# Optimization experiments

Hardware: AMD Instinct MI355X
Metric: run time of the kernel (lower is better)

The kernel has to match this reference:

```python
import jax, jax.numpy as jnp
import numpy as np
from jax import lax

B, C, L = 32, 8, 4096
K, S = 128, 64  # num_shapelets, shapelets_size


def setup_inputs() -> dict:
    key = jax.random.key(0)
    kx, ks = jax.random.split(key)
    x = jax.random.normal(kx, (B, C, L), dtype=jnp.float32)
    shapelets = jax.random.normal(ks, (C, K, S), dtype=jnp.float32)
    return {"x": x, "shapelets": shapelets}


def reference(x, shapelets):
    # x: (B, C, L); shapelets: (C, K, S)
    # Equivalent to: unfold -> cdist(p=2) -> sum over channels -> min over windows.
    # Use the ||a-b||^2 = ||a||^2 + ||b||^2 - 2 a.b expansion so the unfolded
    # (B, C, W, S) tensor is never materialized; cross-terms via grouped conv.
    Bc, Cc, Lc = x.shape
    _, Kc, Sc = shapelets.shape
    dn = ("NCH", "OIH", "NCH")
    # cross[b, c*K+k, w] = sum_s x[b,c,w+s] * shapelets[c,k,s]
    rhs = shapelets.reshape(Cc * Kc, 1, Sc)
    cross = lax.conv_general_dilated(x, rhs, (1,), "VALID",
                                     feature_group_count=Cc,
                                     dimension_numbers=dn)  # (B, C*K, W)
    W = cross.shape[-1]
    cross = cross.reshape(Bc, Cc, Kc, W)
    # sliding window squared norms of x: conv of x^2 with ones kernel per channel
    ones = jnp.ones((Cc, 1, Sc), x.dtype)
    xnorm = lax.conv_general_dilated(x * x, ones, (1,), "VALID",
                                     feature_group_count=Cc,
                                     dimension_numbers=dn)  # (B, C, W)
    snorm = jnp.sum(shapelets * shapelets, axis=-1)  # (C, K)
    d2 = xnorm[:, :, None, :] + snorm[None, :, :, None] - 2.0 * cross  # (B,C,K,W)
    d = jnp.sqrt(jnp.maximum(d2, 1e-12))
    summed = jnp.sum(d, axis=1, keepdims=True)  # (B, 1, K, W)
    return jnp.min(summed, axis=3)  # (B, 1, K)
```

## Files before the change

### kernel.cpp

```cpp
#include <hip/hip_runtime.h>


typedef short short8 __attribute__((ext_vector_type(8)));
typedef float f32x4 __attribute__((ext_vector_type(4)));

constexpr int Bn = 32, Cn = 8, Ln = 4096, Kn = 128, Sn = 64;
constexpr int Wn = Ln - Sn + 1;
constexpr int WT = 128;
constexpr int NWT = (Wn + WT - 1) / WT;
constexpr int BDIM = 256;

__device__ __forceinline__ unsigned int f2bf(float f) {
  unsigned int u = __float_as_uint(f);
  u += 0x7FFFu + ((u >> 16) & 1u);
  return u >> 16;
}

__global__ void prep_kernel(const float* __restrict__ sh,
                            unsigned int* __restrict__ out,
                            unsigned short* __restrict__ hbf,
                            float* __restrict__ snorm) {
  int gid = blockIdx.x * blockDim.x + threadIdx.x;
  out[gid] = 0x7F7FFFFFu;
  if (gid < Cn * Kn) {
    const float4* row = (const float4*)(sh + (size_t)gid * Sn);
    uint2* orow = (uint2*)(hbf + (size_t)gid * Sn);
    float a = 0.f;
    #pragma unroll
    for (int i = 0; i < 16; ++i) {
      float4 v = row[i];
      a += v.x * v.x + v.y * v.y + v.z * v.z + v.w * v.w;
      unsigned int p0 = f2bf(-2.f * v.x) | (f2bf(-2.f * v.y) << 16);
      unsigned int p1 = f2bf(-2.f * v.z) | (f2bf(-2.f * v.w) << 16);
      orow[i] = make_uint2(p0, p1);
    }
    snorm[gid] = a;
  }
}

__launch_bounds__(BDIM, 2)
__global__ void med_kernel(const float* __restrict__ x,
                           const unsigned short* __restrict__ hbf,
                           const float* __restrict__ snorm,
                           unsigned int* __restrict__ out) {
  constexpr int XAS = 204;
  constexpr int XCS = 4 * XAS;
  constexpr int BSS = 80;
  __shared__ __align__(16) unsigned short Xs[Cn * XCS];
  __shared__ __align__(16) unsigned short Bs[Kn * BSS];
  __shared__ __align__(16) float xnormC[Cn * WT];
  __shared__ __align__(16) float snormC[Cn * Kn];
  __shared__ unsigned int smin[Kn];

  const int tid  = threadIdx.x;
  const int b    = blockIdx.y;
  const int w0   = blockIdx.x * WT;
  const int lane = tid & 63;
  const int wv   = tid >> 6;
  const int quad = lane >> 4;
  const int n16  = lane & 15;
  const int wbase = wv * 32;

  const float* xb = x + (size_t)b * Cn * Ln;
  const uint4* hb4 = (const uint4*)hbf;

  uint4 Breg[4];
  #pragma unroll
  for (int rep = 0; rep < 4; ++rep) Breg[rep] = hb4[tid + rep * BDIM];

  {
    const int e = tid;
    const bool act = (e < 196);
    float xv[Cn];
    #pragma unroll
    for (int c = 0; c < Cn; ++c)
      xv[c] = (act && (w0 + e) < Ln) ? xb[c * Ln + w0 + e] : 0.f;
    if (act) {
      #pragma unroll
      for (int c = 0; c < Cn; ++c) {
        unsigned short v = (unsigned short)f2bf(xv[c]);
        #pragma unroll
        for (int r = 0; r < 4; ++r) {
          int t = e - r;
          if (t >= 0) Xs[c * XCS + r * XAS + t] = v;
        }
      }
    }
  }

  ((float4*)snormC)[tid] = ((const float4*)snorm)[tid];
  if (tid < Kn) smin[tid] = 0x7F7FFFFFu;

  {
    int c  = tid >> 5;
    int m0 = (tid & 31) * 4;
    const float* xc = xb + c * Ln;
    auto xq = [&](int i) -> float {
      float v = (i < Ln) ? xc[i] : 0.f;
      return v * v;
    };
    float s0 = 0.f;
    for (int s = 0; s < Sn; ++s) s0 += xq(w0 + m0 + s);
    float s1 = s0 - xq(w0 + m0 + 0) + xq(w0 + m0 + 64);
    float s2 = s1 - xq(w0 + m0 + 1) + xq(w0 + m0 + 65);
    float s3 = s2 - xq(w0 + m0 + 2) + xq(w0 + m0 + 66);
    xnormC[c * WT + m0 + 0] = s0;
    xnormC[c * WT + m0 + 1] = s1;
    xnormC[c * WT + m0 + 2] = s2;
    xnormC[c * WT + m0 + 3] = s3;
  }

  const int r4  = n16 & 3;
  const int t00 = wbase + (n16 & ~3) + quad * 8;
  const int bk  = tid >> 3, bch = tid & 7;

  float dist[2][8][4] = {};

  for (int c = 0; c < Cn; ++c) {
    __syncthreads();

    #pragma unroll
    for (int rep = 0; rep < 4; ++rep)
      *(uint4*)(&Bs[(bk + rep * 32) * BSS + bch * 8]) = Breg[rep];
    __syncthreads();

    if (c < Cn - 1) {
      #pragma unroll
      for (int rep = 0; rep < 4; ++rep)
        Breg[rep] = hb4[(c + 1) * 1024 + tid + rep * BDIM];
    }

    float4 xn[2];
    #pragma unroll
    for (int mt = 0; mt < 2; ++mt)
      xn[mt] = *(const float4*)(&xnormC[c * WT + wbase + mt * 16 + quad * 4]);

    short8 af[2][2];
    #pragma unroll
    for (int mt = 0; mt < 2; ++mt)
      #pragma unroll
      for (int ks = 0; ks < 2; ++ks) {
        const unsigned short* pa = &Xs[c * XCS + r4 * XAS + t00 + mt * 16 + ks * 32];
        uint2 a0 = *(const uint2*)(pa);
        uint2 a1 = *(const uint2*)(pa + 4);
        uint4 q = make_uint4(a0.x, a0.y, a1.x, a1.y);
        af[mt][ks] = __builtin_bit_cast(short8, q);
      }

    #pragma unroll
    for (int nt = 0; nt < 8; ++nt) {
      int ksh = nt * 16 + n16;
      float sn = snormC[c * Kn + ksh];
      short8 b0 = *(const short8*)(&Bs[ksh * BSS + quad * 8]);
      short8 b1 = *(const short8*)(&Bs[ksh * BSS + 32 + quad * 8]);
      #pragma unroll
      for (int mt = 0; mt < 2; ++mt) {
        f32x4 acc;
        #pragma unroll
        for (int rg = 0; rg < 4; ++rg) acc[rg] = xn[mt][rg] + sn;
        acc = __builtin_amdgcn_mfma_f32_16x16x32_bf16(af[mt][0], b0, acc, 0, 0, 0);
        acc = __builtin_amdgcn_mfma_f32_16x16x32_bf16(af[mt][1], b1, acc, 0, 0, 0);
        #pragma unroll
        for (int rg = 0; rg < 4; ++rg)
          dist[mt][nt][rg] += __builtin_amdgcn_sqrtf(acc[rg]);
      }
    }
  }

  const int wql = w0 + wbase + quad * 4;
  #pragma unroll
  for (int nt = 0; nt < 8; ++nt) {
    float v = 3.4e38f;
    #pragma unroll
    for (int mt = 0; mt < 2; ++mt)
      #pragma unroll
      for (int rg = 0; rg < 4; ++rg) {
        int wg = wql + mt * 16 + rg;
        float d = (wg < Wn) ? dist[mt][nt][rg] : 3.4e38f;
        v = fminf(v, d);
      }
    v = fminf(v, __shfl_xor(v, 16, 64));
    v = fminf(v, __shfl_xor(v, 32, 64));
    if (lane < 16)
      atomicMin(&smin[nt * 16 + n16], __float_as_uint(v));
  }
  __syncthreads();
  if (tid < Kn)
    atomicMin(&out[b * Kn + tid], smin[tid]);
}

extern "C" void kernel_launch(void* const* d_in, const int* in_sizes, int n_in,
                              void* d_out, int out_size, void* d_ws, size_t ws_size,
                              hipStream_t stream) {
  const float* x  = (const float*)d_in[0];
  const float* sh = (const float*)d_in[1];
  unsigned int* out = (unsigned int*)d_out;
  unsigned short* hbf = (unsigned short*)d_ws;
  float* snorm = (float*)((char*)d_ws + (size_t)Cn * Kn * Sn * 2);
  hipLaunchKernelGGL(prep_kernel, dim3(16), dim3(256), 0, stream, sh, out, hbf, snorm);
  hipLaunchKernelGGL(med_kernel, dim3(NWT, Bn), dim3(BDIM), 0, stream, x, hbf, snorm, out);
}
```

Baseline: 118.7 us.

## Split shapelets across blocks and keep B fragments in registers over window tiles

```diff
diff --git a/kernel.cpp b/kernel.cpp
--- a/kernel.cpp
+++ b/kernel.cpp
@@ -7,7 +7,9 @@
 constexpr int Bn = 32, Cn = 8, Ln = 4096, Kn = 128, Sn = 64;
 constexpr int Wn = Ln - Sn + 1;
 constexpr int WT = 128;
-constexpr int NWT = (Wn + WT - 1) / WT;
+constexpr int NT = 4;
+constexpr int NCH = 8;
+constexpr int KT = 32;
 constexpr int BDIM = 256;
 
 __device__ __forceinline__ unsigned int f2bf(float f) {
@@ -45,16 +47,14 @@
                            unsigned int* __restrict__ out) {
   constexpr int XAS = 204;
   constexpr int XCS = 4 * XAS;
-  constexpr int BSS = 80;
+  constexpr int XNS = 520;
   __shared__ __align__(16) unsigned short Xs[Cn * XCS];
-  __shared__ __align__(16) unsigned short Bs[Kn * BSS];
-  __shared__ __align__(16) float xnormC[Cn * WT];
-  __shared__ __align__(16) float snormC[Cn * Kn];
-  __shared__ unsigned int smin[Kn];
+  __shared__ __align__(16) float xnormAll[Cn * XNS];
 
   const int tid  = threadIdx.x;
   const int b    = blockIdx.y;
-  const int w0   = blockIdx.x * WT;
+  const int wch0 = blockIdx.x * (WT * NT);
+  const int kh0  = blockIdx.z * KT;
   const int lane = tid & 63;
   const int wv   = tid >> 6;
   const int quad = lane >> 4;
@@ -62,23 +62,54 @@
   const int wbase = wv * 32;
 
   const float* xb = x + (size_t)b * Cn * Ln;
-  const uint4* hb4 = (const uint4*)hbf;
-
-  uint4 Breg[4];
-  #pragma unroll
-  for (int rep = 0; rep < 4; ++rep) Breg[rep] = hb4[tid + rep * BDIM];
 
   {
-    const int e = tid;
-    const bool act = (e < 196);
-    float xv[Cn];
+    int c = tid >> 5;
+    int wl = (tid & 31) * 16;
+    const float* xc = xb + c * Ln;
+    auto xq = [&](int i) -> float {
+      float v = (i < Ln) ? xc[i] : 0.f;
+      return v * v;
+    };
+    int w = wch0 + wl;
+    float s = 0.f;
+    for (int k = 0; k < Sn; ++k) s += xq(w + k);
+    xnormAll[c * XNS + wl] = s;
     #pragma unroll
-    for (int c = 0; c < Cn; ++c)
-      xv[c] = (act && (w0 + e) < Ln) ? xb[c * Ln + w0 + e] : 0.f;
-    if (act) {
+    for (int i = 1; i < 16; ++i) {
+      s += xq(w + Sn - 1 + i) - xq(w + i - 1);
+      xnormAll[c * XNS + wl + i] = s;
+    }
+  }
+
+  short8 Breg[Cn][2][2];
+  float  snB[Cn][2];
+  #pragma unroll
+  for (int c = 0; c < Cn; ++c)
+    #pragma unroll
+    for (int nt = 0; nt < 2; ++nt) {
+      int krow = c * Kn + kh0 + nt * 16 + n16;
+      snB[c][nt] = snorm[krow];
+      #pragma unroll
+      for (int ks = 0; ks < 2; ++ks)
+        Breg[c][nt][ks] = *(const short8*)(hbf + (size_t)krow * Sn + ks * 32 + quad * 8);
+    }
+
+  const int r4  = n16 & 3;
+  const int t00 = wbase + (n16 & ~3) + quad * 8;
+
+  float vmin[2] = {3.4e38f, 3.4e38f};
+
+  for (int tile = 0; tile < NT; ++tile) {
+    const int w0t = wch0 + tile * WT;
+    __syncthreads();
+
+    if (tid < 196) {
+      const int e = tid;
       #pragma unroll
       for (int c = 0; c < Cn; ++c) {
-        unsigned short v = (unsigned short)f2bf(xv[c]);
+        float xv = ((w0t + e) < Ln) ? xb[c * Ln + w0t + e] : 0.f;
+        unsigned short v = (unsigned short)f2bf(xv);
         #pragma unroll
         for (int r = 0; r < 4; ++r) {
           int t = e - r;
@@ -86,107 +117,63 @@
         }
       }
     }
+    __syncthreads();
+
+    float dist[2][2][4] = {};
+
+    #pragma unroll
+    for (int c = 0; c < Cn; ++c) {
+      short8 af[2][2];
+      #pragma unroll
+      for (int mt = 0; mt < 2; ++mt)
+        #pragma unroll
+        for (int ks = 0; ks < 2; ++ks) {
+          const unsigned short* pa = &Xs[c * XCS + r4 * XAS + t00 + mt * 16 + ks * 32];
+          uint2 a0 = *(const uint2*)(pa);
+          uint2 a1 = *(const uint2*)(pa + 4);
+          uint4 q = make_uint4(a0.x, a0.y, a1.x, a1.y);
+          af[mt][ks] = __builtin_bit_cast(short8, q);
+        }
+      float4 xn[2];
+      #pragma unroll
+      for (int mt = 0; mt < 2; ++mt)
+        xn[mt] = *(const float4*)(&xnormAll[c * XNS + tile * WT + wbase + mt * 16 + quad * 4]);
+
+      #pragma unroll
+      for (int nt = 0; nt < 2; ++nt)
+        #pragma unroll
+        for (int mt = 0; mt < 2; ++mt) {
+          f32x4 acc;
+          #pragma unroll
+          for (int rg = 0; rg < 4; ++rg) acc[rg] = xn[mt][rg] + snB[c][nt];
+          acc = __builtin_amdgcn_mfma_f32_16x16x32_bf16(af[mt][0], Breg[c][nt][0], acc, 0, 0, 0);
+          acc = __builtin_amdgcn_mfma_f32_16x16x32_bf16(af[mt][1], Breg[c][nt][1], acc, 0, 0, 0);
+          #pragma unroll
+          for (int rg = 0; rg < 4; ++rg)
+            dist[mt][nt][rg] += __builtin_amdgcn_sqrtf(acc[rg]);
+        }
+    }
+
+    #pragma unroll
+    for (int nt = 0; nt < 2; ++nt)
+      #pragma unroll
+      for (int mt = 0; mt < 2; ++mt)
+        #pragma unroll
+        for (int rg = 0; rg < 4; ++rg) {
+          int wg = w0t + wbase + mt * 16 + quad * 4 + rg;
+          float d = (wg < Wn) ? dist[mt][nt][rg] : 3.4e38f;
+          vmin[nt] = fminf(vmin[nt], d);
+        }
   }
 
-  ((float4*)snormC)[tid] = ((const float4*)snorm)[tid];
-  if (tid < Kn) smin[tid] = 0x7F7FFFFFu;
-
-  {
-    int c  = tid >> 5;
-    int m0 = (tid & 31) * 4;
-    const float* xc = xb + c * Ln;
-    auto xq = [&](int i) -> float {
-      float v = (i < Ln) ? xc[i] : 0.f;
-      return v * v;
-    };
-    float s0 = 0.f;
-    for (int s = 0; s < Sn; ++s) s0 += xq(w0 + m0 + s);
-    float s1 = s0 - xq(w0 + m0 + 0) + xq(w0 + m0 + 64);
-    float s2 = s1 - xq(w0 + m0 + 1) + xq(w0 + m0 + 65);
-    float s3 = s2 - xq(w0 + m0 + 2) + xq(w0 + m0 + 66);
-    xnormC[c * WT + m0 + 0] = s0;
-    xnormC[c * WT + m0 + 1] = s1;
-    xnormC[c * WT + m0 + 2] = s2;
-    xnormC[c * WT + m0 + 3] = s3;
-  }
-
-  const int r4  = n16 & 3;
-  const int t00 = wbase + (n16 & ~3) + quad * 8;
-  const int bk  = tid >> 3, bch = tid & 7;
-
-  float dist[2][8][4] = {};
-
-  for (int c = 0; c < Cn; ++c) {
-    __syncthreads();
-
-    #pragma unroll
-    for (int rep = 0; rep < 4; ++rep)
-      *(uint4*)(&Bs[(bk + rep * 32) * BSS + bch * 8]) = Breg[rep];
-    __syncthreads();
-
-    if (c < Cn - 1) {
-      #pragma unroll
-      for (int rep = 0; rep < 4; ++rep)
-        Breg[rep] = hb4[(c + 1) * 1024 + tid + rep * BDIM];
-    }
-
-    float4 xn[2];
-    #pragma unroll
-    for (int mt = 0; mt < 2; ++mt)
-      xn[mt] = *(const float4*)(&xnormC[c * WT + wbase + mt * 16 + quad * 4]);
-
-    short8 af[2][2];
-    #pragma unroll
-    for (int mt = 0; mt < 2; ++mt)
-      #pragma unroll
-      for (int ks = 0; ks < 2; ++ks) {
-        const unsigned short* pa = &Xs[c * XCS + r4 * XAS + t00 + mt * 16 + ks * 32];
-        uint2 a0 = *(const uint2*)(pa);
-        uint2 a1 = *(const uint2*)(pa + 4);
-        uint4 q = make_uint4(a0.x, a0.y, a1.x, a1.y);
-        af[mt][ks] = __builtin_bit_cast(short8, q);
-      }
-
-    #pragma unroll
-    for (int nt = 0; nt < 8; ++nt) {
-      int ksh = nt * 16 + n16;
-      float sn = snormC[c * Kn + ksh];
-      short8 b0 = *(const short8*)(&Bs[ksh * BSS + quad * 8]);
-      short8 b1 = *(const short8*)(&Bs[ksh * BSS + 32 + quad * 8]);
-      #pragma unroll
-      for (int mt = 0; mt < 2; ++mt) {
-        f32x4 acc;
-        #pragma unroll
-        for (int rg = 0; rg < 4; ++rg) acc[rg] = xn[mt][rg] + sn;
-        acc = __builtin_amdgcn_mfma_f32_16x16x32_bf16(af[mt][0], b0, acc, 0, 0, 0);
-        acc = __builtin_amdgcn_mfma_f32_16x16x32_bf16(af[mt][1], b1, acc, 0, 0, 0);
-        #pragma unroll
-        for (int rg = 0; rg < 4; ++rg)
-          dist[mt][nt][rg] += __builtin_amdgcn_sqrtf(acc[rg]);
-      }
-    }
-  }
-
-  const int wql = w0 + wbase + quad * 4;
   #pragma unroll
-  for (int nt = 0; nt < 8; ++nt) {
-    float v = 3.4e38f;
-    #pragma unroll
-    for (int mt = 0; mt < 2; ++mt)
-      #pragma unroll
-      for (int rg = 0; rg < 4; ++rg) {
-        int wg = wql + mt * 16 + rg;
-        float d = (wg < Wn) ? dist[mt][nt][rg] : 3.4e38f;
-        v = fminf(v, d);
-      }
+  for (int nt = 0; nt < 2; ++nt) {
+    float v = vmin[nt];
     v = fminf(v, __shfl_xor(v, 16, 64));
     v = fminf(v, __shfl_xor(v, 32, 64));
     if (lane < 16)
-      atomicMin(&smin[nt * 16 + n16], __float_as_uint(v));
+      atomicMin(&out[b * Kn + kh0 + nt * 16 + n16], __float_as_uint(v));
   }
-  __syncthreads();
-  if (tid < Kn)
-    atomicMin(&out[b * Kn + tid], smin[tid]);
 }
 
 extern "C" void kernel_launch(void* const* d_in, const int* in_sizes, int n_in,
@@ -198,5 +185,5 @@
   unsigned short* hbf = (unsigned short*)d_ws;
   float* snorm = (float*)((char*)d_ws + (size_t)Cn * Kn * Sn * 2);
   hipLaunchKernelGGL(prep_kernel, dim3(16), dim3(256), 0, stream, sh, out, hbf, snorm);
-  hipLaunchKernelGGL(med_kernel, dim3(NWT, Bn), dim3(BDIM), 0, stream, x, hbf, snorm, out);
+  hipLaunchKernelGGL(med_kernel, dim3(NCH, Bn, Kn / KT), dim3(BDIM), 0, stream, x, hbf, snorm, out);
 }
```

Result: slower. 205.7 us (+73.3%).
